# Performance work log

Hardware: AMD Instinct MI355X
Metric: run time of the kernel (lower is better)

## Reference

```python
import jax, jax.numpy as jnp
import numpy as np

B, N, P, E, H, D, F, L = 16, 500, 100, 128, 8, 16, 512, 6
CLIP = 10.0  # logit_clipping


def _heads(x, h):
    b, n, _ = x.shape
    return x.reshape(b, n, h, -1).transpose(0, 2, 1, 3)  # [b,h,n,d]


def _mha(q, k, v, mask3=None):
    d = q.shape[-1]
    s = jnp.einsum('bhnd,bhmd->bhnm', q, k) / jnp.sqrt(jnp.asarray(d, q.dtype))
    if mask3 is not None:
        s = s + mask3[:, None, :, :]
    w = jax.nn.softmax(s, axis=-1)
    o = jnp.einsum('bhnm,bhmd->bhnd', w, v)
    b, h, n, dd = o.shape
    return o.transpose(0, 2, 1, 3).reshape(b, n, h * dd)


def _ff(x, w1, b1, w2, b2):
    return jax.nn.relu(x @ w1 + b1) @ w2 + b2


def _forward(depot_xy, node_xy, node_demand, load, cur_dist, ninf_mask,
             emb_depot_w, emb_depot_b, emb_node_w, emb_node_b,
             enc_wq, enc_wk, enc_wv, enc_comb_w, enc_comb_b,
             enc_ff1_w, enc_ff1_b, enc_ff2_w, enc_ff2_b,
             dec_wq_last, dec_wk, dec_wv, dec_comb_w, dec_comb_b,
             dec_cap_w, dec_ff1_w, dec_ff1_b, dec_ff2_w, dec_ff2_b,
             current_node):
    # ---------------- encoder ----------------
    node_xy_demand = jnp.concatenate([node_xy, node_demand[:, :, None]], axis=2)  # [B,N,3]
    x = jnp.concatenate([depot_xy @ emb_depot_w + emb_depot_b,
                         node_xy_demand @ emb_node_w + emb_node_b], axis=1)  # [B,N+1,E]
    for i in range(L):
        q = _heads(x @ enc_wq[i], H)
        k = _heads(x @ enc_wk[i], H)
        v = _heads(x @ enc_wv[i], H)
        mh = _mha(q, k, v) @ enc_comb_w[i] + enc_comb_b[i]
        o1 = x + mh
        x = o1 + _ff(o1, enc_ff1_w[i], enc_ff1_b[i], enc_ff2_w[i], enc_ff2_b[i])
    encoded_nodes = x  # [B, N+1, E]
    # decoder kv cache (set_kv)
    k = _heads(encoded_nodes @ dec_wk, H)
    v = _heads(encoded_nodes @ dec_wv, H)
    # ---------------- one decode step ----------------
    encoded_last = jnp.take_along_axis(encoded_nodes, current_node[:, :, None], axis=1)  # [B,P,E]
    input_cat = jnp.concatenate([encoded_last, load[:, :, None]], axis=2)  # [B,P,E+1]
    q = _heads(input_cat @ dec_wq_last, H)
    mh = _mha(q, k, v, mask3=ninf_mask) @ dec_comb_w + dec_comb_b
    mh = mh + encoded_last + load[:, :, None] @ dec_cap_w
    q_ref = _ff(mh, dec_ff1_w, dec_ff1_b, dec_ff2_w, dec_ff2_b) + mh
    score = jnp.einsum('bpe,bne->bpn', q_ref, encoded_nodes) / jnp.sqrt(jnp.asarray(E, q_ref.dtype))
    # distance-based noise injection
    dmin = cur_dist.min(axis=-1, keepdims=True)
    dmax = cur_dist.max(axis=-1, keepdims=True)
    norm_dist = (cur_dist - dmin) / (dmax - dmin + 1e-6)
    problem_size = ninf_mask.shape[2]
    nm = 50.0 / problem_size
    base_noise = jax.random.normal(jax.random.key(42), cur_dist.shape, cur_dist.dtype) * 0.2 + 0.5
    score = score - (1.0 - nm) * jnp.log(norm_dist + 1e-6) + base_noise * nm
    score = CLIP * jnp.tanh(score) + ninf_mask
    return jax.nn.softmax(score, axis=2)  # [B,P,N+1]


def setup_inputs() -> dict:
    key = jax.random.key(0)
    ks = iter(jax.random.split(key, 40))
    def rn(shape, s=0.02):
        return s * jax.random.normal(next(ks), shape, jnp.float32)
    return dict(
        depot_xy=jax.random.uniform(next(ks), (B, 1, 2), jnp.float32),
        node_xy=jax.random.uniform(next(ks), (B, N, 2), jnp.float32),
        node_demand=jax.random.uniform(next(ks), (B, N), jnp.float32),
        load=jax.random.uniform(next(ks), (B, P), jnp.float32),
        cur_dist=jax.random.uniform(next(ks), (B, P, N + 1), jnp.float32),
        ninf_mask=jnp.zeros((B, P, N + 1), jnp.float32),
        current_node=jax.random.randint(next(ks), (B, P), 0, N + 1),
        emb_depot_w=rn((2, E)), emb_depot_b=rn((E,)),
        emb_node_w=rn((3, E)), emb_node_b=rn((E,)),
        enc_wq=rn((L, E, H * D)), enc_wk=rn((L, E, H * D)), enc_wv=rn((L, E, H * D)),
        enc_comb_w=rn((L, H * D, E)), enc_comb_b=rn((L, E)),
        enc_ff1_w=rn((L, E, F)), enc_ff1_b=rn((L, F)),
        enc_ff2_w=rn((L, F, E)), enc_ff2_b=rn((L, E)),
        dec_wq_last=rn((E + 1, H * D)), dec_wk=rn((E, H * D)), dec_wv=rn((E, H * D)),
        dec_comb_w=rn((H * D, E)), dec_comb_b=rn((E,)),
        dec_cap_w=rn((1, E)),
        dec_ff1_w=rn((E, F)), dec_ff1_b=rn((F,)),
        dec_ff2_w=rn((F, E)), dec_ff2_b=rn((E,)),
    )


def reference(depot_xy, node_xy, node_demand, load, cur_dist, ninf_mask, current_node,
              emb_depot_w, emb_depot_b, emb_node_w, emb_node_b,
              enc_wq, enc_wk, enc_wv, enc_comb_w, enc_comb_b,
              enc_ff1_w, enc_ff1_b, enc_ff2_w, enc_ff2_b,
              dec_wq_last, dec_wk, dec_wv, dec_comb_w, dec_comb_b,
              dec_cap_w, dec_ff1_w, dec_ff1_b, dec_ff2_w, dec_ff2_b):
    return _forward(depot_xy, node_xy, node_demand, load, cur_dist, ninf_mask,
                    emb_depot_w, emb_depot_b, emb_node_w, emb_node_b,
                    enc_wq, enc_wk, enc_wv, enc_comb_w, enc_comb_b,
                    enc_ff1_w, enc_ff1_b, enc_ff2_w, enc_ff2_b,
                    dec_wq_last, dec_wk, dec_wv, dec_comb_w, dec_comb_b,
                    dec_cap_w, dec_ff1_w, dec_ff1_b, dec_ff2_w, dec_ff2_b,
                    current_node)
```

## Files before the change

### kernel.cpp

```cpp
#include <hip/hip_runtime.h>
#include <math.h>

#define Bb 16
#define Nn 500
#define NT 501
#define Pp 100
#define Ee 128
#define Hh 8
#define Dd 16
#define Ff 512
#define Ll 6
#define Mtok (Bb*NT)
#define PR (Bb*Pp)
#define TJ 32
#define SPLIT 4
#define KSEG 126
#define DSPLIT 4
#define DSEG 126
#define ENCP (6*128*384)
#define DECP (128*256)

__global__ __launch_bounds__(256) void pack_k(
    const float* __restrict__ ewq, const float* __restrict__ ewk, const float* __restrict__ ewv,
    const float* __restrict__ dwk, const float* __restrict__ dwv,
    float* __restrict__ encP, float* __restrict__ decP)
{
  int i = blockIdx.x*256 + threadIdx.x;
  if (i < ENCP) {
    int l = i / (128*384); int rem = i - l*128*384; int k = rem / 384; int n = rem - k*384;
    float v;
    if (n < 128)      v = ewq[((size_t)l*128 + k)*128 + n];
    else if (n < 256) v = ewk[((size_t)l*128 + k)*128 + (n-128)];
    else              v = ewv[((size_t)l*128 + k)*128 + (n-256)];
    encP[i] = v;
  } else {
    int j = i - ENCP;
    if (j < DECP) {
      int k = j >> 8; int n = j & 255;
      decP[j] = (n < 128) ? dwk[k*128 + n] : dwv[k*128 + (n-128)];
    }
  }
}

__global__ __launch_bounds__(256) void embed_k(
    const float* __restrict__ depot_xy, const float* __restrict__ node_xy,
    const float* __restrict__ node_demand,
    const float* __restrict__ wD, const float* __restrict__ bD,
    const float* __restrict__ wN, const float* __restrict__ bN,
    float* __restrict__ x)
{
  int t = blockIdx.x*256 + threadIdx.x;
  if (t >= Mtok*Ee) return;
  int e   = t & (Ee-1);
  int tok = t >> 7;
  int b   = tok / NT;
  int n   = tok - b*NT;
  float v;
  if (n == 0) {
    v = depot_xy[b*2+0]*wD[0*Ee+e] + depot_xy[b*2+1]*wD[1*Ee+e] + bD[e];
  } else {
    int nn = n - 1;
    float c0 = node_xy[(b*Nn + nn)*2 + 0];
    float c1 = node_xy[(b*Nn + nn)*2 + 1];
    float c2 = node_demand[b*Nn + nn];
    v = c0*wN[0*Ee+e] + c1*wN[1*Ee+e] + c2*wN[2*Ee+e] + bN[e];
  }
  x[(size_t)tok*Ee + e] = v;
}

__global__ __launch_bounds__(256) void gemm_k(
    const float* __restrict__ A, const float* __restrict__ W,
    const float* __restrict__ bias, const float* __restrict__ res,
    float* __restrict__ C, int M, int N, int K, int relu)
{
  __shared__ __align__(16) float As[2][16][64];
  __shared__ __align__(16) float Bs[2][16][64];
  int tid = threadIdx.x;
  int tx = tid & 15, ty = tid >> 4;
  int m0 = blockIdx.x * 64, n0 = blockIdx.y * 64;
  float acc[4][4];
  #pragma unroll
  for (int i=0;i<4;i++)
    #pragma unroll
    for (int j=0;j<4;j++) acc[i][j] = 0.f;

  int ar = tid >> 2;
  int ak = (tid & 3) << 2;
  int br = tid >> 4;
  int bc = (tid & 15) << 2;

  const float* Ap = A + (size_t)(m0 + ar)*K + ak;
  const float* Wp = W + (size_t)br*N + n0 + bc;
  bool aok = (m0 + ar) < M;

  float4 av = aok ? *(const float4*)(Ap) : make_float4(0.f,0.f,0.f,0.f);
  float4 wv = *(const float4*)(Wp);

  int nk = K >> 4;
  for (int t = 0; t < nk; ++t) {
    int cur = t & 1;
    As[cur][ak+0][ar] = av.x; As[cur][ak+1][ar] = av.y;
    As[cur][ak+2][ar] = av.z; As[cur][ak+3][ar] = av.w;
    *(float4*)(&Bs[cur][br][bc]) = wv;
    __syncthreads();
    if (t+1 < nk) {
      av = aok ? *(const float4*)(Ap + (t+1)*16) : make_float4(0.f,0.f,0.f,0.f);
      wv = *(const float4*)(Wp + (size_t)(t+1)*16*N);
    }
    #pragma unroll
    for (int k=0;k<16;k++){
      float4 a4 = *(const float4*)(&As[cur][k][ty*4]);
      float4 b4 = *(const float4*)(&Bs[cur][k][tx*4]);
      float avv[4] = {a4.x,a4.y,a4.z,a4.w};
      float bvv[4] = {b4.x,b4.y,b4.z,b4.w};
      #pragma unroll
      for (int i=0;i<4;i++)
        #pragma unroll
        for (int j=0;j<4;j++)
          acc[i][j] = fmaf(avv[i], bvv[j], acc[i][j]);
    }
  }

  float4 bv = make_float4(0.f,0.f,0.f,0.f);
  if (bias) bv = *(const float4*)(bias + n0 + tx*4);
  #pragma unroll
  for (int i=0;i<4;i++){
    int row = m0 + ty*4 + i;
    if (row >= M) continue;
    float4 o;
    o.x = acc[i][0] + bv.x; o.y = acc[i][1] + bv.y;
    o.z = acc[i][2] + bv.z; o.w = acc[i][3] + bv.w;
    if (relu){ o.x=fmaxf(o.x,0.f); o.y=fmaxf(o.y,0.f); o.z=fmaxf(o.z,0.f); o.w=fmaxf(o.w,0.f); }
    if (res){
      float4 rv = *(const float4*)(res + (size_t)row*N + n0 + tx*4);
      o.x += rv.x; o.y += rv.y; o.z += rv.z; o.w += rv.w;
    }
    *(float4*)(C + (size_t)row*N + n0 + tx*4) = o;
  }
}

__device__ __forceinline__ float dot4(float4 a, float4 b){
  return fmaf(a.x,b.x, fmaf(a.y,b.y, fmaf(a.z,b.z, a.w*b.w)));
}

__global__ __launch_bounds__(256) void attn_enc_k(
    const float* __restrict__ QKV, float* __restrict__ part_o,
    float* __restrict__ part_l)
{
  int blk = blockIdx.x;
  int s  = blk % SPLIT;
  int cc = blk / SPLIT;
  int c  = cc & 1;
  int bh = cc >> 1;
  int h  = bh & (Hh-1);
  int b  = bh >> 3;
  int p  = c*256 + (int)threadIdx.x;
  const int klo = s*KSEG;
  int kseg = NT - klo; if (kseg > KSEG) kseg = KSEG;

  __shared__ __align__(16) float4 Ks[2][TJ][4];
  __shared__ __align__(16) float4 Vs[2][TJ][4];

  int tid = threadIdx.x;
  int row = (tid >> 2) & 31;
  int lc  = tid & 3;
  bool isV = tid >= 128;
  const int kvoff = isV ? 256 : 128;

  float4 q0,q1,q2,q3;
  if (p < NT) {
    const float4* qp = (const float4*)(QKV + ((size_t)(b*NT + p))*384 + h*Dd);
    q0=qp[0]; q1=qp[1]; q2=qp[2]; q3=qp[3];
  } else {
    q0=q1=q2=q3=make_float4(0,0,0,0);
  }

  if (row < kseg) {
    float4 v = *((const float4*)(QKV + ((size_t)(b*NT + klo + row))*384 + kvoff + h*Dd) + lc);
    if (isV) Vs[0][row][lc] = v; else Ks[0][row][lc] = v;
  }
  __syncthreads();

  float l = 0.f;
  float4 o0=make_float4(0,0,0,0), o1=o0, o2=o0, o3=o0;
  const int ntiles = (kseg + TJ - 1)/TJ;
  int buf = 0;

  for (int t = 0; t < ntiles; ++t) {
    int j0 = t*TJ;
    if (t+1 < ntiles) {
      int jj = j0 + TJ + row;
      if (jj < kseg) {
        float4 v = *((const float4*)(QKV + ((size_t)(b*NT + klo + jj))*384 + kvoff + h*Dd) + lc);
        if (isV) Vs[buf^1][row][lc] = v; else Ks[buf^1][row][lc] = v;
      }
    }
    int jend = kseg - j0; if (jend > TJ) jend = TJ;

    if (p < NT) {
      #pragma unroll 4
      for (int jj=0;jj<jend;jj++){
        const float4* kr = &Ks[buf][jj][0];
        float s0 = (dot4(q0,kr[0])+dot4(q1,kr[1])) + (dot4(q2,kr[2])+dot4(q3,kr[3]));
        float w = __expf(s0 * 0.25f);
        l += w;
        const float4* vr = &Vs[buf][jj][0];
        float4 v0=vr[0],v1=vr[1],v2=vr[2],v3=vr[3];
        o0.x=fmaf(w,v0.x,o0.x); o0.y=fmaf(w,v0.y,o0.y); o0.z=fmaf(w,v0.z,o0.z); o0.w=fmaf(w,v0.w,o0.w);
        o1.x=fmaf(w,v1.x,o1.x); o1.y=fmaf(w,v1.y,o1.y); o1.z=fmaf(w,v1.z,o1.z); o1.w=fmaf(w,v1.w,o1.w);
        o2.x=fmaf(w,v2.x,o2.x); o2.y=fmaf(w,v2.y,o2.y); o2.z=fmaf(w,v2.z,o2.z); o2.w=fmaf(w,v2.w,o2.w);
        o3.x=fmaf(w,v3.x,o3.x); o3.y=fmaf(w,v3.y,o3.y); o3.z=fmaf(w,v3.z,o3.z); o3.w=fmaf(w,v3.w,o3.w);
      }
    }
    __syncthreads();
    buf ^= 1;
  }

  if (p < NT) {
    size_t rbase = ((size_t)s*128 + bh)*NT + p;
    float4* po = (float4*)(part_o + rbase*16);
    po[0]=o0; po[1]=o1; po[2]=o2; po[3]=o3;
    part_l[rbase] = l;
  }
}

__global__ __launch_bounds__(256) void attn_comb_k(
    const float* __restrict__ part_o, const float* __restrict__ part_l,
    float* __restrict__ O)
{
  int t = blockIdx.x*256 + threadIdx.x;
  if (t >= 128*NT*16) return;
  int d  = t & 15;
  int rq = t >> 4;
  int q  = rq % NT;
  int bh = rq / NT;
  int h = bh & 7, b = bh >> 3;
  const size_t R = (size_t)128*NT;
  float L = 0.f, o = 0.f;
  #pragma unroll
  for (int s=0;s<SPLIT;s++){
    L += part_l[(size_t)s*R + rq];
    o += part_o[((size_t)s*R + rq)*16 + d];
  }
  O[((size_t)(b*NT + q))*Ee + h*Dd + d] = o / L;
}

__global__ __launch_bounds__(128) void attn_dec_k(
    const float* __restrict__ Q, const float* __restrict__ KV,
    const float* __restrict__ mask,
    float* __restrict__ part_o, float* __restrict__ part_l)
{
  int blk = blockIdx.x;
  int s  = blk & (DSPLIT-1);
  int bh = blk >> 2;
  int h  = bh & (Hh-1);
  int b  = bh >> 3;
  int klo = s*DSEG;
  int kn  = NT - klo; if (kn > DSEG) kn = DSEG;

  __shared__ __align__(16) float4 Ks[DSEG][4];
  __shared__ __align__(16) float4 Vs[DSEG][4];

  int tid = threadIdx.x;
  for (int i = tid; i < kn*8; i += 128) {
    int row  = i >> 3;
    int q8   = i & 7;
    int quad = q8 & 3;
    int isv  = q8 >> 2;
    float4 v = *(const float4*)(KV + ((size_t)(b*NT + klo + row))*256 + isv*128 + h*Dd + quad*4);
    if (isv) Vs[row][quad] = v; else Ks[row][quad] = v;
  }
  __syncthreads();

  int p = tid;
  if (p >= Pp) return;
  int r = b*Pp + p;
  const float4* qp = (const float4*)(Q + (size_t)r*Ee + h*Dd);
  float4 qa=qp[0], qb=qp[1], qc=qp[2], qd=qp[3];
  const float* mrow = mask + (size_t)r*NT + klo;

  float l = 0.f;
  float4 o0=make_float4(0,0,0,0), o1=o0, o2=o0, o3=o0;
  for (int j=0;j<kn;++j){
    float sc = (dot4(qa,Ks[j][0])+dot4(qb,Ks[j][1])) + (dot4(qc,Ks[j][2])+dot4(qd,Ks[j][3]));
    float w = __expf(sc*0.25f + mrow[j]);
    l += w;
    float4 v0=Vs[j][0],v1=Vs[j][1],v2=Vs[j][2],v3=Vs[j][3];
    o0.x=fmaf(w,v0.x,o0.x); o0.y=fmaf(w,v0.y,o0.y); o0.z=fmaf(w,v0.z,o0.z); o0.w=fmaf(w,v0.w,o0.w);
    o1.x=fmaf(w,v1.x,o1.x); o1.y=fmaf(w,v1.y,o1.y); o1.z=fmaf(w,v1.z,o1.z); o1.w=fmaf(w,v1.w,o1.w);
    o2.x=fmaf(w,v2.x,o2.x); o2.y=fmaf(w,v2.y,o2.y); o2.z=fmaf(w,v2.z,o2.z); o2.w=fmaf(w,v2.w,o2.w);
    o3.x=fmaf(w,v3.x,o3.x); o3.y=fmaf(w,v3.y,o3.y); o3.z=fmaf(w,v3.z,o3.z); o3.w=fmaf(w,v3.w,o3.w);
  }

  size_t rb = ((size_t)s*PR + r)*Hh + h;
  float4* po = (float4*)(part_o + rb*16);
  po[0]=o0; po[1]=o1; po[2]=o2; po[3]=o3;
  part_l[rb] = l;
}

__global__ __launch_bounds__(256) void attn_dcomb_k(
    const float* __restrict__ part_o, const float* __restrict__ part_l,
    float* __restrict__ O)
{
  int t = blockIdx.x*256 + threadIdx.x;
  if (t >= PR*Ee) return;
  int d = t & 15;
  int h = (t >> 4) & 7;
  int r = t >> 7;
  const size_t S = (size_t)PR*Hh;
  size_t rb = (size_t)r*Hh + h;
  float L = 0.f, o = 0.f;
  #pragma unroll
  for (int s=0;s<DSPLIT;s++){
    L += part_l[(size_t)s*S + rb];
    o += part_o[((size_t)s*S + rb)*16 + d];
  }
  O[(size_t)r*Ee + h*Dd + d] = o / L;
}

__global__ __launch_bounds__(256) void gather_k(
    const float* __restrict__ x, const int* __restrict__ cur, float* __restrict__ encl)
{
  int t = blockIdx.x*256 + threadIdx.x;
  if (t >= PR*Ee) return;
  int e = t & (Ee-1);
  int r = t >> 7;
  int b = r / Pp;
  int node = cur[r];
  encl[(size_t)r*Ee + e] = x[((size_t)(b*NT + node))*Ee + e];
}

__global__ __launch_bounds__(128) void decq_k(
    const float* __restrict__ encl, const float* __restrict__ loadv,
    const float* __restrict__ Wq, float* __restrict__ q)
{
  __shared__ float row[Ee];
  int r = blockIdx.x, e = threadIdx.x;
  row[e] = encl[(size_t)r*Ee + e];
  __syncthreads();
  float acc = 0.f;
  #pragma unroll 4
  for (int k=0;k<Ee;k++) acc = fmaf(row[k], Wq[k*128 + e], acc);
  acc = fmaf(loadv[r], Wq[Ee*128 + e], acc);
  q[(size_t)r*128 + e] = acc;
}

__global__ __launch_bounds__(128) void dec_comb_k(
    const float* __restrict__ att, const float* __restrict__ W,
    const float* __restrict__ bias, const float* __restrict__ encl,
    const float* __restrict__ loadv, const float* __restrict__ capw,
    float* __restrict__ mh)
{
  __shared__ float row[Ee];
  int r = blockIdx.x, e = threadIdx.x;
  row[e] = att[(size_t)r*Ee + e];
  __syncthreads();
  float acc = 0.f;
  #pragma unroll 4
  for (int k=0;k<Ee;k++) acc = fmaf(row[k], W[k*Ee + e], acc);
  mh[(size_t)r*Ee + e] = acc + bias[e] + encl[(size_t)r*Ee + e] + loadv[r]*capw[e];
}

__global__ __launch_bounds__(128) void score_k(
    const float* __restrict__ qref, const float* __restrict__ x, float* __restrict__ score)
{
  __shared__ float q[Ee];
  int r = blockIdx.x;
  int b = r / Pp;
  q[threadIdx.x] = qref[(size_t)r*Ee + threadIdx.x];
  __syncthreads();
  for (int n = threadIdx.x; n < NT; n += 128){
    const float4* xr = (const float4*)(x + ((size_t)(b*NT + n))*Ee);
    float acc = 0.f;
    #pragma unroll
    for (int k=0;k<Ee/4;k++){
      float4 xv = xr[k];
      const float* qq = &q[k*4];
      acc = fmaf(qq[0],xv.x, fmaf(qq[1],xv.y, fmaf(qq[2],xv.z, fmaf(qq[3],xv.w, acc))));
    }
    score[(size_t)r*NT + n] = acc * 0.08838834764831845f;
  }
}

__device__ __forceinline__ unsigned rotl32(unsigned x, int r){ return (x<<r)|(x>>(32-r)); }

__device__ float tf_normal(unsigned idx)
{
  unsigned x0 = 0u;
  unsigned x1 = idx;
  const unsigned ks[3] = {0u, 42u, 0u ^ 42u ^ 0x1BD11BDAu};
  x0 += ks[0]; x1 += ks[1];
  const int rotA[4] = {13,15,26,6};
  const int rotB[4] = {17,29,16,24};
  #pragma unroll
  for (int i=0;i<5;i++){
    #pragma unroll
    for (int q=0;q<4;q++){
      int rr = (i&1) ? rotB[q] : rotA[q];
      x0 += x1; x1 = rotl32(x1, rr); x1 ^= x0;
    }
    x0 += ks[(i+1)%3];
    x1 += ks[(i+2)%3] + (unsigned)(i+1);
  }
  unsigned bits = x0 ^ x1;
  float f = __uint_as_float((bits >> 9) | 0x3f800000u) - 1.0f;
  const float lo = -0.99999994f;
  float u = f * 2.0f + lo;
  u = fmaxf(lo, u);
  float w = -log1pf(-u*u);
  float p;
  if (w < 5.0f) {
    w -= 2.5f;
    p = 2.81022636e-08f;
    p = fmaf(p, w, 3.43273939e-07f);
    p = fmaf(p, w, -3.5233877e-06f);
    p = fmaf(p, w, -4.39150654e-06f);
    p = fmaf(p, w, 0.00021858087f);
    p = fmaf(p, w, -0.00125372503f);
    p = fmaf(p, w, -0.00417768164f);
    p = fmaf(p, w, 0.246640727f);
    p = fmaf(p, w, 1.50140941f);
  } else {
    w = sqrtf(w) - 3.0f;
    p = -0.000200214257f;
    p = fmaf(p, w, 0.000100950558f);
    p = fmaf(p, w, 0.00134934322f);
    p = fmaf(p, w, -0.00367342844f);
    p = fmaf(p, w, 0.00573950773f);
    p = fmaf(p, w, -0.0076224613f);
    p = fmaf(p, w, 0.00943887047f);
    p = fmaf(p, w, 1.00167406f);
    p = fmaf(p, w, 2.83297682f);
  }
  return 1.4142135623730951f * (p * u);
}

__global__ __launch_bounds__(512) void final_k(
    const float* __restrict__ score, const float* __restrict__ cur_dist,
    const float* __restrict__ ninf, float* __restrict__ out)
{
  __shared__ float red[512];
  const float NM = (float)(50.0/501.0);
  const float C1 = (float)(1.0 - 50.0/501.0);
  int r = blockIdx.x;
  int t = threadIdx.x;
  float cd = 0.f, dmn = 1e30f, dmx = -1e30f;
  if (t < NT) { cd = cur_dist[(size_t)r*NT + t]; dmn = cd; dmx = cd; }
  red[t] = dmn; __syncthreads();
  for (int s=256;s>0;s>>=1){ if (t<s) red[t]=fminf(red[t],red[t+s]); __syncthreads(); }
  float dmin = red[0]; __syncthreads();
  red[t] = dmx; __syncthreads();
  for (int s=256;s>0;s>>=1){ if (t<s) red[t]=fmaxf(red[t],red[t+s]); __syncthreads(); }
  float dmax = red[0]; __syncthreads();

  float sval = -1e30f;
  if (t < NT) {
    float nd = (cd - dmin) / (dmax - dmin + 1e-6f);
    float z  = tf_normal((unsigned)r*501u + (unsigned)t);
    float s  = score[(size_t)r*NT + t] - C1*logf(nd + 1e-6f) + (z*0.2f + 0.5f)*NM;
    sval = 10.0f*tanhf(s) + ninf[(size_t)r*NT + t];
  }
  red[t] = sval; __syncthreads();
  for (int s=256;s>0;s>>=1){ if (t<s) red[t]=fmaxf(red[t],red[t+s]); __syncthreads(); }
  float smax = red[0]; __syncthreads();
  float e = (t < NT) ? expf(sval - smax) : 0.f;
  red[t] = e; __syncthreads();
  for (int s=256;s>0;s>>=1){ if (t<s) red[t]+=red[t+s]; __syncthreads(); }
  float ssum = red[0];
  if (t < NT) out[(size_t)r*NT + t] = e / ssum;
}

extern "C" void kernel_launch(void* const* d_in, const int* in_sizes, int n_in,
                              void* d_out, int out_size, void* d_ws, size_t ws_size,
                              hipStream_t stream)
{
  (void)in_sizes; (void)n_in; (void)out_size; (void)ws_size;
  const float* depot_xy    = (const float*)d_in[0];
  const float* node_xy     = (const float*)d_in[1];
  const float* node_demand = (const float*)d_in[2];
  const float* loadv       = (const float*)d_in[3];
  const float* cur_dist    = (const float*)d_in[4];
  const float* ninf        = (const float*)d_in[5];
  const int*   cur_node    = (const int*)d_in[6];
  const float* emb_depot_w = (const float*)d_in[7];
  const float* emb_depot_b = (const float*)d_in[8];
  const float* emb_node_w  = (const float*)d_in[9];
  const float* emb_node_b  = (const float*)d_in[10];
  const float* enc_wq      = (const float*)d_in[11];
  const float* enc_wk      = (const float*)d_in[12];
  const float* enc_wv      = (const float*)d_in[13];
  const float* enc_comb_w  = (const float*)d_in[14];
  const float* enc_comb_b  = (const float*)d_in[15];
  const float* enc_ff1_w   = (const float*)d_in[16];
  const float* enc_ff1_b   = (const float*)d_in[17];
  const float* enc_ff2_w   = (const float*)d_in[18];
  const float* enc_ff2_b   = (const float*)d_in[19];
  const float* dec_wq_last = (const float*)d_in[20];
  const float* dec_wk      = (const float*)d_in[21];
  const float* dec_wv      = (const float*)d_in[22];
  const float* dec_comb_w  = (const float*)d_in[23];
  const float* dec_comb_b  = (const float*)d_in[24];
  const float* dec_cap_w   = (const float*)d_in[25];
  const float* dec_ff1_w   = (const float*)d_in[26];
  const float* dec_ff1_b   = (const float*)d_in[27];
  const float* dec_ff2_w   = (const float*)d_in[28];
  const float* dec_ff2_b   = (const float*)d_in[29];

  float* ws = (float*)d_ws;
  const size_t SZ = (size_t)Mtok*Ee;
  float* xb    = ws + 0*SZ;
  float* qkvb  = ws + 1*SZ;
  float* atb   = ws + 4*SZ;
  float* o1b   = ws + 5*SZ;
  float* ffb   = ws + 6*SZ;
  float* encPk = ws + 10*SZ;
  float* decPk = encPk + ENCP;
  float* part_o = ffb;
  float* part_l = o1b;
  float* dpart_o = ffb;
  float* dpart_l = o1b;
  float* encl  = qkvb + 2*SZ;
  float* qdec  = encl + 204800;
  float* attd  = qdec + 204800;
  float* mhb   = attd + 204800;
  float* qrefb = atb;
  float* ffh2  = ffb;
  float* scoreb= o1b;

  pack_k<<<(ENCP + DECP + 255)/256, 256, 0, stream>>>(
      enc_wq, enc_wk, enc_wv, dec_wk, dec_wv, encPk, decPk);

  embed_k<<<(Mtok*Ee + 255)/256, 256, 0, stream>>>(
      depot_xy, node_xy, node_demand, emb_depot_w, emb_depot_b,
      emb_node_w, emb_node_b, xb);

  dim3 gqkv((Mtok + 63)/64, 384/64);
  dim3 g128((Mtok + 63)/64, Ee/64);
  dim3 gff ((Mtok + 63)/64, Ff/64);
  const int gcomb = (128*NT*16 + 255)/256;
  for (int l = 0; l < Ll; ++l) {
    gemm_k<<<gqkv, 256, 0, stream>>>(xb, encPk + (size_t)l*128*384, nullptr, nullptr, qkvb, Mtok, 384, Ee, 0);
    attn_enc_k<<<Bb*Hh*2*SPLIT, 256, 0, stream>>>(qkvb, part_o, part_l);
    attn_comb_k<<<gcomb, 256, 0, stream>>>(part_o, part_l, atb);
    gemm_k<<<g128, 256, 0, stream>>>(atb, enc_comb_w + (size_t)l*Ee*Ee, enc_comb_b + l*Ee, xb, o1b, Mtok, Ee, Ee, 0);
    gemm_k<<<gff, 256, 0, stream>>>(o1b, enc_ff1_w + (size_t)l*Ee*Ff, enc_ff1_b + l*Ff, nullptr, ffb, Mtok, Ff, Ee, 1);
    gemm_k<<<g128, 256, 0, stream>>>(ffb, enc_ff2_w + (size_t)l*Ff*Ee, enc_ff2_b + l*Ee, o1b, xb, Mtok, Ee, Ff, 0);
  }

  dim3 gkv((Mtok + 63)/64, 256/64);
  gemm_k<<<gkv, 256, 0, stream>>>(xb, decPk, nullptr, nullptr, qkvb, Mtok, 256, Ee, 0);
  gather_k<<<(PR*Ee + 255)/256, 256, 0, stream>>>(xb, cur_node, encl);
  decq_k<<<PR, 128, 0, stream>>>(encl, loadv, dec_wq_last, qdec);
  attn_dec_k<<<Bb*Hh*DSPLIT, 128, 0, stream>>>(qdec, qkvb, ninf, dpart_o, dpart_l);
  attn_dcomb_k<<<(PR*Ee + 255)/256, 256, 0, stream>>>(dpart_o, dpart_l, attd);
  dec_comb_k<<<PR, 128, 0, stream>>>(attd, dec_comb_w, dec_comb_b, encl, loadv, dec_cap_w, mhb);
  dim3 gd1((PR + 63)/64, Ff/64);
  gemm_k<<<gd1, 256, 0, stream>>>(mhb, dec_ff1_w, dec_ff1_b, nullptr, ffh2, PR, Ff, Ee, 1);
  dim3 gd2((PR + 63)/64, Ee/64);
  gemm_k<<<gd2, 256, 0, stream>>>(ffh2, dec_ff2_w, dec_ff2_b, mhb, qrefb, PR, Ee, Ff, 0);
  score_k<<<PR, 128, 0, stream>>>(qrefb, xb, scoreb);
  final_k<<<PR, 512, 0, stream>>>(scoreb, cur_dist, ninf, (float*)d_out);
}
```

Before: 968.5 us.

## Batch decoder scoring as tiled GEMM, pad GEMM LDS, use wave-shuffle softmax reductions

```diff
diff --git a/kernel.cpp b/kernel.cpp
--- a/kernel.cpp
+++ b/kernel.cpp
@@ -19,6 +19,7 @@
 #define DSEG 126
 #define ENCP (6*128*384)
 #define DECP (128*256)
+#define SNP 512
 
 __global__ __launch_bounds__(256) void pack_k(
     const float* __restrict__ ewq, const float* __restrict__ ewk, const float* __restrict__ ewv,
@@ -73,8 +74,8 @@
     const float* __restrict__ bias, const float* __restrict__ res,
     float* __restrict__ C, int M, int N, int K, int relu)
 {
-  __shared__ __align__(16) float As[2][16][64];
-  __shared__ __align__(16) float Bs[2][16][64];
+  __shared__ __align__(16) float As[2][16][68];
+  __shared__ __align__(16) float Bs[2][16][68];
   int tid = threadIdx.x;
   int tx = tid & 15, ty = tid >> 4;
   int m0 = blockIdx.x * 64, n0 = blockIdx.y * 64;
@@ -361,24 +362,96 @@
   mh[(size_t)r*Ee + e] = acc + bias[e] + encl[(size_t)r*Ee + e] + loadv[r]*capw[e];
 }
 
-__global__ __launch_bounds__(128) void score_k(
-    const float* __restrict__ qref, const float* __restrict__ x, float* __restrict__ score)
-{
-  __shared__ float q[Ee];
-  int r = blockIdx.x;
-  int b = r / Pp;
-  q[threadIdx.x] = qref[(size_t)r*Ee + threadIdx.x];
-  __syncthreads();
-  for (int n = threadIdx.x; n < NT; n += 128){
-    const float4* xr = (const float4*)(x + ((size_t)(b*NT + n))*Ee);
-    float acc = 0.f;
+__global__ __launch_bounds__(256) void xt_k(
+    const float* __restrict__ x, float* __restrict__ xT)
+{
+  __shared__ float T[32][33];
+  int n0 = blockIdx.x * 32;
+  int k0 = blockIdx.y * 32;
+  int b  = blockIdx.z;
+  int t  = threadIdx.x;
+  int row = t >> 3;
+  int c4  = (t & 7) << 2;
+
+  int n = n0 + row;
+  float4 v = make_float4(0.f,0.f,0.f,0.f);
+  if (n < NT) v = *(const float4*)(x + ((size_t)(b*NT + n))*Ee + k0 + c4);
+  T[c4+0][row] = v.x; T[c4+1][row] = v.y; T[c4+2][row] = v.z; T[c4+3][row] = v.w;
+  __syncthreads();
+
+  const float SC = 0.08838834764831845f;
+  float4 o;
+  o.x = T[row][c4+0]*SC; o.y = T[row][c4+1]*SC;
+  o.z = T[row][c4+2]*SC; o.w = T[row][c4+3]*SC;
+  *(float4*)(xT + ((size_t)(b*Ee + k0 + row))*SNP + n0 + c4) = o;
+}
+
+__global__ __launch_bounds__(256) void score_gemm_k(
+    const float* __restrict__ qref, const float* __restrict__ xT,
+    float* __restrict__ score)
+{
+  __shared__ __align__(16) float As[2][16][68];
+  __shared__ __align__(16) float Bs[2][16][68];
+  int tid = threadIdx.x;
+  int tx = tid & 15, ty = tid >> 4;
+  int m0 = blockIdx.x * 64;
+  int n0 = blockIdx.y * 64;
+  int b  = blockIdx.z;
+
+  const float* A = qref + (size_t)b*Pp*Ee;
+  const float* W = xT   + (size_t)b*Ee*SNP;
+  float*       C = score + (size_t)b*Pp*SNP;
+
+  float acc[4][4];
+  #pragma unroll
+  for (int i=0;i<4;i++)
     #pragma unroll
-    for (int k=0;k<Ee/4;k++){
-      float4 xv = xr[k];
-      const float* qq = &q[k*4];
-      acc = fmaf(qq[0],xv.x, fmaf(qq[1],xv.y, fmaf(qq[2],xv.z, fmaf(qq[3],xv.w, acc))));
-    }
-    score[(size_t)r*NT + n] = acc * 0.08838834764831845f;
+    for (int j=0;j<4;j++) acc[i][j] = 0.f;
+
+  int ar = tid >> 2;
+  int ak = (tid & 3) << 2;
+  int br = tid >> 4;
+  int bc = (tid & 15) << 2;
+
+  const float* Ap = A + (size_t)(m0 + ar)*Ee + ak;
+  const float* Wp = W + (size_t)br*SNP + n0 + bc;
+  bool aok = (m0 + ar) < Pp;
+
+  float4 av = aok ? *(const float4*)(Ap) : make_float4(0.f,0.f,0.f,0.f);
+  float4 wv = *(const float4*)(Wp);
+
+  for (int t = 0; t < 8; ++t) {
+    int cur = t & 1;
+    As[cur][ak+0][ar] = av.x; As[cur][ak+1][ar] = av.y;
+    As[cur][ak+2][ar] = av.z; As[cur][ak+3][ar] = av.w;
+    *(float4*)(&Bs[cur][br][bc]) = wv;
+    __syncthreads();
+    if (t+1 < 8) {
+      av = aok ? *(const float4*)(Ap + (t+1)*16) : make_float4(0.f,0.f,0.f,0.f);
+      wv = *(const float4*)(Wp + (size_t)(t+1)*16*SNP);
+    }
+    #pragma unroll
+    for (int k=0;k<16;k++){
+      float4 a4 = *(const float4*)(&As[cur][k][ty*4]);
+      float4 b4 = *(const float4*)(&Bs[cur][k][tx*4]);
+      float avv[4] = {a4.x,a4.y,a4.z,a4.w};
+      float bvv[4] = {b4.x,b4.y,b4.z,b4.w};
+      #pragma unroll
+      for (int i=0;i<4;i++)
+        #pragma unroll
+        for (int j=0;j<4;j++)
+          acc[i][j] = fmaf(avv[i], bvv[j], acc[i][j]);
+    }
+    __syncthreads();
+  }
+
+  #pragma unroll
+  for (int i=0;i<4;i++){
+    int row = m0 + ty*4 + i;
+    if (row >= Pp) continue;
+    float4 o;
+    o.x = acc[i][0]; o.y = acc[i][1]; o.z = acc[i][2]; o.w = acc[i][3];
+    *(float4*)(C + (size_t)row*SNP + n0 + tx*4) = o;
   }
 }
 
@@ -439,34 +512,53 @@
     const float* __restrict__ score, const float* __restrict__ cur_dist,
     const float* __restrict__ ninf, float* __restrict__ out)
 {
-  __shared__ float red[512];
+  __shared__ float smn[8], smx[8], sm2[8], ss[8];
   const float NM = (float)(50.0/501.0);
   const float C1 = (float)(1.0 - 50.0/501.0);
   int r = blockIdx.x;
   int t = threadIdx.x;
-  float cd = 0.f, dmn = 1e30f, dmx = -1e30f;
-  if (t < NT) { cd = cur_dist[(size_t)r*NT + t]; dmn = cd; dmx = cd; }
-  red[t] = dmn; __syncthreads();
-  for (int s=256;s>0;s>>=1){ if (t<s) red[t]=fminf(red[t],red[t+s]); __syncthreads(); }
-  float dmin = red[0]; __syncthreads();
-  red[t] = dmx; __syncthreads();
-  for (int s=256;s>0;s>>=1){ if (t<s) red[t]=fmaxf(red[t],red[t+s]); __syncthreads(); }
-  float dmax = red[0]; __syncthreads();
+  int wid = t >> 6, lane = t & 63;
+
+  float cd = 0.f;
+  float mn = 1e30f, mx = -1e30f;
+  if (t < NT) { cd = cur_dist[(size_t)r*NT + t]; mn = cd; mx = cd; }
+  #pragma unroll
+  for (int off=32; off>=1; off>>=1){
+    mn = fminf(mn, __shfl_xor(mn, off));
+    mx = fmaxf(mx, __shfl_xor(mx, off));
+  }
+  if (lane == 0){ smn[wid] = mn; smx[wid] = mx; }
+  __syncthreads();
+  float dmin = smn[0], dmax = smx[0];
+  #pragma unroll
+  for (int i=1;i<8;i++){ dmin = fminf(dmin, smn[i]); dmax = fmaxf(dmax, smx[i]); }
 
   float sval = -1e30f;
   if (t < NT) {
     float nd = (cd - dmin) / (dmax - dmin + 1e-6f);
     float z  = tf_normal((unsigned)r*501u + (unsigned)t);
-    float s  = score[(size_t)r*NT + t] - C1*logf(nd + 1e-6f) + (z*0.2f + 0.5f)*NM;
+    float s  = score[(size_t)r*SNP + t] - C1*logf(nd + 1e-6f) + (z*0.2f + 0.5f)*NM;
     sval = 10.0f*tanhf(s) + ninf[(size_t)r*NT + t];
   }
-  red[t] = sval; __syncthreads();
-  for (int s=256;s>0;s>>=1){ if (t<s) red[t]=fmaxf(red[t],red[t+s]); __syncthreads(); }
-  float smax = red[0]; __syncthreads();
+  float mv = sval;
+  #pragma unroll
+  for (int off=32; off>=1; off>>=1) mv = fmaxf(mv, __shfl_xor(mv, off));
+  if (lane == 0) sm2[wid] = mv;
+  __syncthreads();
+  float smax = sm2[0];
+  #pragma unroll
+  for (int i=1;i<8;i++) smax = fmaxf(smax, sm2[i]);
+
   float e = (t < NT) ? expf(sval - smax) : 0.f;
-  red[t] = e; __syncthreads();
-  for (int s=256;s>0;s>>=1){ if (t<s) red[t]+=red[t+s]; __syncthreads(); }
-  float ssum = red[0];
+  float sv = e;
+  #pragma unroll
+  for (int off=32; off>=1; off>>=1) sv += __shfl_xor(sv, off);
+  if (lane == 0) ss[wid] = sv;
+  __syncthreads();
+  float ssum = ss[0];
+  #pragma unroll
+  for (int i=1;i<8;i++) ssum += ss[i];
+
   if (t < NT) out[(size_t)r*NT + t] = e / ssum;
 }
 
@@ -525,6 +617,7 @@
   float* mhb   = attd + 204800;
   float* qrefb = atb;
   float* ffh2  = ffb;
+  float* xTb   = ffb;
   float* scoreb= o1b;
 
   pack_k<<<(ENCP + DECP + 255)/256, 256, 0, stream>>>(
@@ -558,6 +651,9 @@
   gemm_k<<<gd1, 256, 0, stream>>>(mhb, dec_ff1_w, dec_ff1_b, nullptr, ffh2, PR, Ff, Ee, 1);
   dim3 gd2((PR + 63)/64, Ee/64);
   gemm_k<<<gd2, 256, 0, stream>>>(ffh2, dec_ff2_w, dec_ff2_b, mhb, qrefb, PR, Ee, Ff, 0);
-  score_k<<<PR, 128, 0, stream>>>(qrefb, xb, scoreb);
+  dim3 gxt(16, 4, 16);
+  xt_k<<<gxt, 256, 0, stream>>>(xb, xTb);
+  dim3 gsc(2, 8, 16);
+  score_gemm_k<<<gsc, 256, 0, stream>>>(qrefb, xTb, scoreb);
   final_k<<<PR, 512, 0, stream>>>(scoreb, cur_dist, ninf, (float*)d_out);
 }
```

Result: faster. 909.5 us (-6.1%).
